# Performance work log

Measured on AMD Instinct MI355X. Metric: run time of the kernel, lower is better.

## Reference

```python
import jax, jax.numpy as jnp
import numpy as np

DIM = 128
K = 4
B, H, W = 2, 256, 256
DEFORM_WEIGHT = 0.3


def conv2d(x, w, b, pad):
    # x [B,C,H,W], w [O,I,kh,kw], stride 1
    y = jax.lax.conv_general_dilated(
        x, w, (1, 1), [(pad, pad), (pad, pad)],
        dimension_numbers=('NCHW', 'OIHW', 'NCHW'))
    return y + b[None, :, None, None]


def gelu(x):
    return jax.nn.gelu(x, approximate=False)  # torch nn.GELU default (erf)


def grid_sample_k(feat, grid):
    """Bilinear grid_sample, padding_mode='border', align_corners=True.
    feat: [B,C,H,W]; grid: [B,K,H,W,2] (x,y) in [-1,1]. Returns [B,C,K,H,W]."""
    Bn, C, Hh, Ww = feat.shape
    px = (grid[..., 0] + 1.0) * 0.5 * (Ww - 1)
    py = (grid[..., 1] + 1.0) * 0.5 * (Hh - 1)
    px = jnp.clip(px, 0.0, Ww - 1)
    py = jnp.clip(py, 0.0, Hh - 1)
    x0 = jnp.floor(px).astype(jnp.int32)
    y0 = jnp.floor(py).astype(jnp.int32)
    x1 = jnp.minimum(x0 + 1, Ww - 1)
    y1 = jnp.minimum(y0 + 1, Hh - 1)
    wx = (px - x0)[:, None]  # [B,1,K,H,W]
    wy = (py - y0)[:, None]
    featf = feat.reshape(Bn, C, Hh * Ww)

    def gather(yi, xi):
        idx = (yi * Ww + xi).reshape(Bn, -1)  # [B, K*H*W]
        g = jax.vmap(lambda f, i: f[:, i])(featf, idx)  # [B,C,K*H*W]
        return g.reshape(Bn, C, *yi.shape[1:])

    v00 = gather(y0, x0)
    v01 = gather(y0, x1)
    v10 = gather(y1, x0)
    v11 = gather(y1, x1)
    return (v00 * (1 - wx) * (1 - wy) + v01 * wx * (1 - wy)
            + v10 * (1 - wx) * wy + v11 * wx * wy)


def setup_inputs() -> dict:
    key = jax.random.key(0)
    ks = jax.random.split(key, 16)
    nrm = lambda k, shape, s: jax.random.normal(k, shape, dtype=jnp.float32) * s
    return {
        'query_feat': jax.random.normal(ks[0], (B, DIM, H, W), dtype=jnp.float32),
        'key_feat': jax.random.normal(ks[1], (B, DIM, H, W), dtype=jnp.float32),
        # offset_net: Conv(dim,dim,3) -> GELU -> Conv(dim,2K,3); small scale keeps offsets sane
        'ow1': nrm(ks[2], (DIM, DIM, 3, 3), 0.02), 'ob1': jnp.zeros((DIM,), jnp.float32),
        'ow2': nrm(ks[3], (2 * K, DIM, 3, 3), 0.01), 'ob2': jnp.zeros((2 * K,), jnp.float32),
        # weight_net: Conv(dim,dim//4,3) -> GELU -> Conv(dim//4,K,1)
        'ww1': nrm(ks[4], (DIM // 4, DIM, 3, 3), 0.05), 'wb1': jnp.zeros((DIM // 4,), jnp.float32),
        'ww2': nrm(ks[5], (K, DIM // 4, 1, 1), 0.05), 'wb2': jnp.zeros((K,), jnp.float32),
        # fusion_conv: Conv(dim,dim,1) -> GELU -> Conv(dim,dim,1)
        'fw1': nrm(ks[6], (DIM, DIM, 1, 1), 0.05), 'fb1': jnp.zeros((DIM,), jnp.float32),
        'fw2': nrm(ks[7], (DIM, DIM, 1, 1), 0.05), 'fb2': jnp.zeros((DIM,), jnp.float32),
    }


def reference(query_feat, key_feat, ow1, ob1, ow2, ob2, ww1, wb1, ww2, wb2,
              fw1, fb1, fw2, fb2):
    offsets = conv2d(gelu(conv2d(query_feat, ow1, ob1, 1)), ow2, ob2, 1)  # [B,2K,H,W]
    wlog = conv2d(gelu(conv2d(query_feat, ww1, wb1, 1)), ww2, wb2, 0)     # [B,K,H,W]
    Bn, C, Hh, Ww = key_feat.shape
    Kp = wlog.shape[1]
    off = offsets.reshape(Bn, Kp, 2, Hh, Ww).transpose(0, 1, 3, 4, 2)  # [B,K,H,W,2]
    gy, gx = jnp.meshgrid(jnp.linspace(-1.0, 1.0, Hh),
                          jnp.linspace(-1.0, 1.0, Ww), indexing='ij')
    base = jnp.stack([gx, gy], axis=-1).astype(off.dtype)  # [H,W,2] (x,y)
    scale = jnp.array([Ww / 2.0, Hh / 2.0], dtype=off.dtype)
    grid = jnp.clip(base + off / scale, -1.0, 1.0)  # [B,K,H,W,2]
    sampled = grid_sample_k(key_feat, grid)  # [B,C,K,H,W]
    wsoft = jax.nn.softmax(wlog, axis=1)[:, None]  # [B,1,K,H,W]
    agg = (sampled * wsoft).sum(axis=2)  # [B,C,H,W]
    fused = conv2d(gelu(conv2d(agg, fw1, fb1, 0)), fw2, fb2, 0)
    return query_feat + fused * DEFORM_WEIGHT
```

## Files before the change

kernel.cpp:

```cpp
#include <hip/hip_runtime.h>
#include <hip/hip_fp16.h>

typedef unsigned short u16;
typedef __attribute__((ext_vector_type(8))) short bf16x8;
typedef __attribute__((ext_vector_type(4))) float f32x4;

constexpr int B_ = 2, C_ = 128, H_ = 256, W_ = 256, P_ = H_ * W_;
constexpr int HP_ = 258, WP_ = 258;

union HU { __half2 h; unsigned int u; };

__device__ __forceinline__ float bf2f(u16 u) {
  union { unsigned int i; float f; } v; v.i = ((unsigned int)u) << 16; return v.f;
}
__device__ __forceinline__ u16 f2bf(float f) {
  union { float f; unsigned int i; } v; v.f = f;
  return (u16)((v.i + 0x7fffu + ((v.i >> 16) & 1u)) >> 16);
}
__device__ __forceinline__ float gelu_f(float x) {
  float u = x * (1.5957691216057308f + 0.071354816272f * x * x);
  return x / (1.0f + __expf(-u));
}

__device__ __forceinline__ void async16(const u16* g, u16* l) {
  __builtin_amdgcn_global_load_lds(
      (const __attribute__((address_space(1))) unsigned int*)g,
      (__attribute__((address_space(3))) unsigned int*)l, 16, 0, 0);
}

__global__ __launch_bounds__(256) void border_zero(u16* __restrict__ buf) {
  int idx = blockIdx.x * 256 + threadIdx.x;
  int c = idx & 127;
  int t = idx >> 7;
  int pos = t % 258;
  int side = (t / 258) & 3;
  int b = t / (258 * 4);
  int h, w;
  if (side == 0) { h = 0;   w = pos; }
  else if (side == 1) { h = 257; w = pos; }
  else if (side == 2) { h = pos; w = 0; }
  else { h = pos; w = 257; }
  buf[(((size_t)b * HP_ + h) * WP_ + w) * C_ + c] = 0;
}

__global__ __launch_bounds__(256) void to_nhwc(const float* __restrict__ in, u16* __restrict__ out,
                                               int OHp, int OWp, int opad) {
  __shared__ u16 l[64 * 66];
  int tid = threadIdx.x;
  int b = blockIdx.z >> 1, c0 = (blockIdx.z & 1) * 64;
  int h = blockIdx.y, w0 = blockIdx.x * 64;
  for (int it = 0; it < 16; ++it) {
    int lin = it * 256 + tid;
    int c = lin >> 6, w = lin & 63;
    l[c * 66 + w] = f2bf(in[(((size_t)b * C_ + c0 + c) * H_ + h) * W_ + w0 + w]);
  }
  __syncthreads();
  for (int it = 0; it < 16; ++it) {
    int lin = it * 256 + tid;
    int w = lin >> 6, c = lin & 63;
    out[(((size_t)b * OHp + h + opad) * OWp + (w0 + w + opad)) * C_ + c0 + c] = l[c * 66 + w];
  }
}

__global__ __launch_bounds__(256) void repack_weights(
    const float* __restrict__ ow1, const float* __restrict__ ow2,
    const float* __restrict__ ww1, const float* __restrict__ fw1,
    const float* __restrict__ fw2, u16* __restrict__ wb) {
  int idx = blockIdx.x * 256 + threadIdx.x;
  float v;
  if (idx < 184320) {
    int e = idx & 7, lr = (idx >> 3) & 15, kb = (idx >> 7) & 3;
    int t = idx >> 9;
    int g = t % 10, u = t / 10;
    int cq = u & 3, tap = u >> 2;
    int ci = cq * 32 + kb * 8 + e, co = g * 16 + lr;
    v = (co < 128) ? ow1[(co * 128 + ci) * 9 + tap]
                   : ww1[((co - 128) * 128 + ci) * 9 + tap];
  } else if (idx < 202752) {
    int j = idx - 184320;
    int e = j & 7, lr = (j >> 3) & 15, kb = (j >> 7) & 3;
    int cq = (j >> 9) & 3, tap = j >> 11;
    int ci = cq * 32 + kb * 8 + e, co = lr;
    v = (co < 8) ? ow2[(co * 128 + ci) * 9 + tap] : 0.0f;
  } else if (idx < 219136) {
    v = fw1[idx - 202752];
  } else {
    v = fw2[idx - 219136];
  }
  wb[idx] = f2bf(v);
}

template <int BM, int BN, int WR, int WC, int GT, int EPI>
__global__ __launch_bounds__(256) void gemm_conv3(
    const u16* __restrict__ A, const u16* __restrict__ Wf,
    const float* __restrict__ bias1, const float* __restrict__ bias2,
    u16* __restrict__ outb, u16* __restrict__ outw, float* __restrict__ outf) {
  constexpr int TM = BM / WR / 16, TN = BN / WC / 16;
  constexpr int RP = BM + 16;
  constexpr int CHR = RP * 4;
  __shared__ __align__(16) u16 As[3 * RP * 32];
  const int tid = threadIdx.x, lane = tid & 63, wave = tid >> 6;
  const int id = blockIdx.x;
  const int s = id >> 3;
  const int h = ((id & 7) << 5) | (s & 31);
  const int w0 = ((s >> 5) & 1) * BM;
  const int b = (s >> 6) & 1;
  const int wm = (wave / WC) * (BM / WR), wn = (wave % WC) * (BN / WC);
  const int lr = lane & 15, kq = lane >> 4;
  const int gbase = wn >> 4;

  int preA[TM][3];
#pragma unroll
  for (int i = 0; i < TM; i++)
#pragma unroll
    for (int kx = 0; kx < 3; kx++) {
      int row = wm + i * 16 + lr + kx;
      preA[i][kx] = row * 64 + (((kq ^ (row >> 1)) & 3) << 4);
    }

  f32x4 acc[TM][TN];
#pragma unroll
  for (int i = 0; i < TM; i++)
#pragma unroll
    for (int j = 0; j < TN; j++) { f32x4 z = {0.f, 0.f, 0.f, 0.f}; acc[i][j] = z; }

  const size_t rowpx = ((size_t)b * HP_ + h) * WP_ + w0;
  for (int cq = 0; cq < 4; ++cq) {
    const int ci0 = cq * 32;
    __syncthreads();
    for (int i = tid; i < 3 * CHR; i += 256) {
      int ky = i / CHR;
      int rem = i - ky * CHR;
      int px = rem >> 2, cb = rem & 3;
      async16(A + (rowpx + (size_t)ky * WP_ + px) * 128 + ci0 + (((cb ^ (px >> 1)) & 3) << 3),
              As + i * 8);
    }
    __syncthreads();
#pragma unroll
    for (int tap = 0; tap < 9; ++tap) {
      const int ky = tap / 3, kx = tap % 3;
      bf16x8 bfr[TN], af[TM];
#pragma unroll
      for (int j = 0; j < TN; ++j)
        bfr[j] = *(const bf16x8*)&Wf[(size_t)((((tap * 4 + cq) * GT + gbase + j) * 4 + kq) * 16 + lr) * 8];
#pragma unroll
      for (int i = 0; i < TM; ++i)
        af[i] = *(const bf16x8*)((const char*)As + ky * (RP * 64) + preA[i][kx]);
#pragma unroll
      for (int i = 0; i < TM; i++)
#pragma unroll
        for (int j = 0; j < TN; j++)
          acc[i][j] = __builtin_amdgcn_mfma_f32_16x16x32_bf16(af[i], bfr[j], acc[i][j], 0, 0, 0);
    }
  }

#pragma unroll
  for (int i = 0; i < TM; i++) {
#pragma unroll
    for (int j = 0; j < TN; j++) {
      const int co = wn + j * 16 + lr;
#pragma unroll
      for (int r = 0; r < 4; r++) {
        const int w = w0 + wm + i * 16 + (lane >> 4) * 4 + r;
        float v = acc[i][j][r];
        if (EPI == 3) {
          if (co < 128) {
            v = gelu_f(v + bias1[co]);
            outb[(((size_t)b * HP_ + h + 1) * WP_ + (w + 1)) * 128 + co] = f2bf(v);
          } else {
            v = gelu_f(v + bias2[co - 128]);
            outw[((size_t)b * P_ + (size_t)h * W_ + w) * 32 + (co - 128)] = f2bf(v);
          }
        } else {
          if (co < 8)
            outf[((size_t)b * P_ + (size_t)h * W_ + w) * 8 + co] = v + bias1[co];
        }
      }
    }
  }
}

template <int BM, int BN, int WR, int WC, int EPI>
__global__ __launch_bounds__(256) void gemm_conv(
    const u16* __restrict__ A, const u16* __restrict__ Wt,
    const float* __restrict__ bias,
    u16* __restrict__ outb, float* __restrict__ outf,
    const float* __restrict__ resid) {
  constexpr int TM = BM / WR / 16, TN = BN / WC / 16;
  __shared__ __align__(16) u16 As[BM * 64];
  __shared__ __align__(16) u16 Bs[BN * 64];
  const int tid = threadIdx.x, lane = tid & 63, wave = tid >> 6;
  const int h = blockIdx.y, w0 = blockIdx.x * BM;
  const int b = blockIdx.z;
  const int wr = wave / WC, wc = wave % WC;
  const int wm = wr * (BM / WR), wn = wc * (BN / WC);
  const int lr = lane & 15;
  const int sw = (lr & 7);

  f32x4 acc[TM][TN];
#pragma unroll
  for (int i = 0; i < TM; i++)
#pragma unroll
    for (int j = 0; j < TN; j++) { f32x4 z = {0.f, 0.f, 0.f, 0.f}; acc[i][j] = z; }

  for (int c = 0; c < 2; ++c) {
    const int ci0 = c << 6;
    const u16* Ab = A + (((size_t)b * H_ + h) * W_ + w0) * 128 + ci0;
    const u16* Wb = Wt + ci0;
    __syncthreads();
    for (int i = tid; i < BM * 8; i += 256) {
      int r = i >> 3, cb = i & 7;
      async16(Ab + r * 128 + ((cb ^ (r & 7)) << 3), As + i * 8);
    }
    for (int i = tid; i < BN * 8; i += 256) {
      int r = i >> 3, cb = i & 7;
      async16(Wb + r * 128 + ((cb ^ (r & 7)) << 3), Bs + i * 8);
    }
    __syncthreads();
#pragma unroll
    for (int ks = 0; ks < 2; ++ks) {
      const int kb = ks * 4 + (lane >> 4);
      bf16x8 af[TM], bfr[TN];
#pragma unroll
      for (int i = 0; i < TM; i++)
        af[i] = *(const bf16x8*)&As[(wm + i * 16 + lr) * 64 + ((kb ^ sw) << 3)];
#pragma unroll
      for (int j = 0; j < TN; j++)
        bfr[j] = *(const bf16x8*)&Bs[(wn + j * 16 + lr) * 64 + ((kb ^ sw) << 3)];
#pragma unroll
      for (int i = 0; i < TM; i++)
#pragma unroll
        for (int j = 0; j < TN; j++)
          acc[i][j] = __builtin_amdgcn_mfma_f32_16x16x32_bf16(af[i], bfr[j], acc[i][j], 0, 0, 0);
    }
  }

#pragma unroll
  for (int i = 0; i < TM; i++) {
#pragma unroll
    for (int j = 0; j < TN; j++) {
      const int co = wn + j * 16 + lr;
      if (EPI == 2) {
        const int w = w0 + wm + i * 16 + (lane >> 4) * 4;
        size_t idx = ((size_t)b * 128 + co) * (size_t)P_ + (size_t)h * W_ + w;
        float4 rv = *(const float4*)&resid[idx];
        float bi = bias[co];
        float4 ov;
        ov.x = rv.x + 0.3f * (acc[i][j][0] + bi);
        ov.y = rv.y + 0.3f * (acc[i][j][1] + bi);
        ov.z = rv.z + 0.3f * (acc[i][j][2] + bi);
        ov.w = rv.w + 0.3f * (acc[i][j][3] + bi);
        *(float4*)&outf[idx] = ov;
      } else {
#pragma unroll
        for (int r = 0; r < 4; r++) {
          const int w = w0 + wm + i * 16 + (lane >> 4) * 4 + r;
          float v = gelu_f(acc[i][j][r] + bias[co]);
          outb[(((size_t)b * H_ + h) * W_ + w) * 128 + co] = f2bf(v);
        }
      }
    }
  }
}

__global__ __launch_bounds__(256) void prep(
    const float* __restrict__ offs, const u16* __restrict__ w1,
    const float* __restrict__ ww2, const float* __restrict__ wb2,
    uint4* __restrict__ desc) {
  const int pix = blockIdx.x * 256 + threadIdx.x;
  const int p = pix & 65535, h = p >> 8, w = p & 255;
  const u16* wp = w1 + (size_t)pix * 32;
  float f[32];
#pragma unroll
  for (int i = 0; i < 32; i += 2) {
    unsigned int u = *(const unsigned int*)&wp[i];
    f[i] = bf2f((u16)u); f[i + 1] = bf2f((u16)(u >> 16));
  }
  float lg[4];
#pragma unroll
  for (int k = 0; k < 4; k++) {
    float s = wb2[k];
#pragma unroll
    for (int i = 0; i < 32; i++) s = fmaf(ww2[k * 32 + i], f[i], s);
    lg[k] = s;
  }
  float mx = fmaxf(fmaxf(lg[0], lg[1]), fmaxf(lg[2], lg[3]));
  float e[4], sum = 0.f;
#pragma unroll
  for (int k = 0; k < 4; k++) { e[k] = __expf(lg[k] - mx); sum += e[k]; }
  const float inv = 1.0f / sum;

  const float* op = offs + (size_t)pix * 8;
#pragma unroll
  for (int k = 0; k < 4; k++) {
    float gx = (2.0f * w / 255.0f - 1.0f) + op[2 * k] * (1.0f / 128.0f);
    float gy = (2.0f * h / 255.0f - 1.0f) + op[2 * k + 1] * (1.0f / 128.0f);
    gx = fminf(fmaxf(gx, -1.f), 1.f);
    gy = fminf(fmaxf(gy, -1.f), 1.f);
    float px = fminf(fmaxf((gx + 1.f) * 127.5f, 0.f), 255.f);
    float py = fminf(fmaxf((gy + 1.f) * 127.5f, 0.f), 255.f);
    int x0 = (int)px, y0 = (int)py;
    int x1 = min(x0 + 1, 255), y1 = min(y0 + 1, 255);
    float wx = px - x0, wy = py - y0;
    float wk = e[k] * inv;
    float w00 = (1.f - wx) * (1.f - wy) * wk, w01 = wx * (1.f - wy) * wk;
    float w10 = (1.f - wx) * wy * wk,         w11 = wx * wy * wk;
    HU t01, t23;
    t01.h = __floats2half2_rn(w00, w01);
    t23.h = __floats2half2_rn(w10, w11);
    uint4 d;
    d.x = (unsigned)(y0 * 256 + x0) | ((unsigned)(x1 - x0) << 16) | ((unsigned)(y1 - y0) << 17);
    d.y = t01.u; d.z = t23.u; d.w = 0;
    desc[(size_t)pix * 4 + k] = d;
  }
}

__global__ __launch_bounds__(256) void sampler(
    const uint4* __restrict__ desc, const u16* __restrict__ keyn, u16* __restrict__ agg) {
  const int tid = threadIdx.x, lane = tid & 63, wv = tid >> 6;
  const int pix = blockIdx.x * 4 + wv;
  const int b = pix >> 16;
  const u16* kb = keyn + (size_t)b * (P_ * C_) + 2 * lane;
  float a0 = 0.f, a1 = 0.f;
#pragma unroll
  for (int k = 0; k < 4; ++k) {
    uint4 d = desc[(size_t)pix * 4 + k];
    const int boff = (int)(d.x & 0xFFFFu) << 7;
    const int o01 = (int)((d.x >> 16) & 1u) << 7;
    const int o10 = (int)((d.x >> 17) & 1u) << 15;
    const u16* c0 = kb + boff;
    unsigned u00 = *(const unsigned*)(c0);
    unsigned u01 = *(const unsigned*)(c0 + o01);
    unsigned u10 = *(const unsigned*)(c0 + o10);
    unsigned u11 = *(const unsigned*)(c0 + o10 + o01);
    HU t01, t23; t01.u = d.y; t23.u = d.z;
    float2 wA = __half22float2(t01.h);
    float2 wB = __half22float2(t23.h);
    a0 = fmaf(wA.x, bf2f((u16)u00), a0);
    a0 = fmaf(wA.y, bf2f((u16)u01), a0);
    a0 = fmaf(wB.x, bf2f((u16)u10), a0);
    a0 = fmaf(wB.y, bf2f((u16)u11), a0);
    a1 = fmaf(wA.x, bf2f((u16)(u00 >> 16)), a1);
    a1 = fmaf(wA.y, bf2f((u16)(u01 >> 16)), a1);
    a1 = fmaf(wB.x, bf2f((u16)(u10 >> 16)), a1);
    a1 = fmaf(wB.y, bf2f((u16)(u11 >> 16)), a1);
  }
  unsigned outu = ((unsigned)f2bf(a1) << 16) | (unsigned)f2bf(a0);
  *(unsigned*)&agg[(size_t)pix * C_ + 2 * lane] = outu;
}

extern "C" void kernel_launch(void* const* d_in, const int* in_sizes, int n_in,
                              void* d_out, int out_size, void* d_ws, size_t ws_size,
                              hipStream_t stream) {
  (void)in_sizes; (void)n_in; (void)out_size; (void)ws_size;
  const float* q   = (const float*)d_in[0];
  const float* key = (const float*)d_in[1];
  const float* ow1 = (const float*)d_in[2];
  const float* ob1 = (const float*)d_in[3];
  const float* ow2 = (const float*)d_in[4];
  const float* ob2 = (const float*)d_in[5];
  const float* ww1 = (const float*)d_in[6];
  const float* wb1 = (const float*)d_in[7];
  const float* ww2 = (const float*)d_in[8];
  const float* wb2 = (const float*)d_in[9];
  const float* fw1 = (const float*)d_in[10];
  const float* fb1 = (const float*)d_in[11];
  const float* fw2 = (const float*)d_in[12];
  const float* fb2 = (const float*)d_in[13];
  float* out = (float*)d_out;
  char* ws = (char*)d_ws;

  u16* qpad   = (u16*)(ws);
  u16* t1pad  = (u16*)(ws + 34080768);
  u16* keyn   = (u16*)(ws + 68161536);
  float* offs = (float*)(ws + 101715968);
  u16* w1b    = (u16*)(ws + 105910272);
  u16* wbuf   = (u16*)(ws + 114298880);
  u16* t2  = qpad;
  u16* agg = t1pad;
  uint4* desc = (uint4*)(ws + 16777216);

  border_zero<<<1032, 256, 0, stream>>>(qpad);
  border_zero<<<1032, 256, 0, stream>>>(t1pad);
  repack_weights<<<920, 256, 0, stream>>>(ow1, ow2, ww1, fw1, fw2, wbuf);
  to_nhwc<<<dim3(4, 256, 4), 256, 0, stream>>>(q, qpad, HP_, WP_, 1);
  to_nhwc<<<dim3(4, 256, 4), 256, 0, stream>>>(key, keyn, H_, W_, 0);

  gemm_conv3<128, 160, 2, 2, 10, 3><<<1024, 256, 0, stream>>>(
      qpad, wbuf, ob1, wb1, t1pad, w1b, nullptr);
  gemm_conv3<128, 16, 4, 1, 1, 1><<<1024, 256, 0, stream>>>(
      t1pad, wbuf + 184320, ob2, nullptr, nullptr, nullptr, offs);
  prep<<<512, 256, 0, stream>>>(offs, w1b, ww2, wb2, desc);
  sampler<<<32768, 256, 0, stream>>>(desc, keyn, agg);
  gemm_conv<128, 128, 2, 2, 0><<<dim3(2, 256, 2), 256, 0, stream>>>(
      agg, wbuf + 202752, fb1, t2, nullptr, nullptr);
  gemm_conv<128, 128, 2, 2, 2><<<dim3(2, 256, 2), 256, 0, stream>>>(
      t2, wbuf + 219136, fb2, nullptr, out, q);
}
```

Before: 397.5 us.

## Fuse prologue kernels, retile 3x3 conv, fuse offset conv with prep and 1x1 pair

Merges border zeroing, NHWC conversion and weight repacking into one launch. Retiles the big 3x3 conv to 4-row by 32-pixel tiles so halo rows are reused across output rows. Fuses the offset conv with the softmax/descriptor prep through LDS, removing the fp32 offsets round trip. Fuses both 1x1 convs so the GELU intermediate stays in LDS instead of global memory. The larger LDS footprint may lower occupancy.

```diff
diff --git a/kernel.cpp b/kernel.cpp
--- a/kernel.cpp
+++ b/kernel.cpp
@@ -28,273 +28,259 @@
       (__attribute__((address_space(3))) unsigned int*)l, 16, 0, 0);
 }
 
-__global__ __launch_bounds__(256) void border_zero(u16* __restrict__ buf) {
-  int idx = blockIdx.x * 256 + threadIdx.x;
-  int c = idx & 127;
-  int t = idx >> 7;
-  int pos = t % 258;
-  int side = (t / 258) & 3;
-  int b = t / (258 * 4);
-  int h, w;
-  if (side == 0) { h = 0;   w = pos; }
-  else if (side == 1) { h = 257; w = pos; }
-  else if (side == 2) { h = pos; w = 0; }
-  else { h = pos; w = 257; }
-  buf[(((size_t)b * HP_ + h) * WP_ + w) * C_ + c] = 0;
-}
-
-__global__ __launch_bounds__(256) void to_nhwc(const float* __restrict__ in, u16* __restrict__ out,
-                                               int OHp, int OWp, int opad) {
-  __shared__ u16 l[64 * 66];
-  int tid = threadIdx.x;
-  int b = blockIdx.z >> 1, c0 = (blockIdx.z & 1) * 64;
-  int h = blockIdx.y, w0 = blockIdx.x * 64;
-  for (int it = 0; it < 16; ++it) {
-    int lin = it * 256 + tid;
-    int c = lin >> 6, w = lin & 63;
-    l[c * 66 + w] = f2bf(in[(((size_t)b * C_ + c0 + c) * H_ + h) * W_ + w0 + w]);
-  }
-  __syncthreads();
-  for (int it = 0; it < 16; ++it) {
-    int lin = it * 256 + tid;
-    int w = lin >> 6, c = lin & 63;
-    out[(((size_t)b * OHp + h + opad) * OWp + (w0 + w + opad)) * C_ + c0 + c] = l[c * 66 + w];
-  }
-}
-
-__global__ __launch_bounds__(256) void repack_weights(
+__global__ __launch_bounds__(256) void prologue(
+    const float* __restrict__ q, const float* __restrict__ key,
     const float* __restrict__ ow1, const float* __restrict__ ow2,
     const float* __restrict__ ww1, const float* __restrict__ fw1,
-    const float* __restrict__ fw2, u16* __restrict__ wb) {
-  int idx = blockIdx.x * 256 + threadIdx.x;
-  float v;
-  if (idx < 184320) {
-    int e = idx & 7, lr = (idx >> 3) & 15, kb = (idx >> 7) & 3;
-    int t = idx >> 9;
-    int g = t % 10, u = t / 10;
-    int cq = u & 3, tap = u >> 2;
-    int ci = cq * 32 + kb * 8 + e, co = g * 16 + lr;
-    v = (co < 128) ? ow1[(co * 128 + ci) * 9 + tap]
-                   : ww1[((co - 128) * 128 + ci) * 9 + tap];
-  } else if (idx < 202752) {
-    int j = idx - 184320;
-    int e = j & 7, lr = (j >> 3) & 15, kb = (j >> 7) & 3;
-    int cq = (j >> 9) & 3, tap = j >> 11;
-    int ci = cq * 32 + kb * 8 + e, co = lr;
-    v = (co < 8) ? ow2[(co * 128 + ci) * 9 + tap] : 0.0f;
-  } else if (idx < 219136) {
-    v = fw1[idx - 202752];
+    const float* __restrict__ fw2,
+    u16* __restrict__ qpad, u16* __restrict__ keyn, u16* __restrict__ t1pad,
+    u16* __restrict__ wb) {
+  __shared__ u16 l[64 * 66];
+  const int id = blockIdx.x, tid = threadIdx.x;
+  if (id < 8192) {
+    int z = id >> 10, r = id & 1023;
+    int bx = r & 3, by = r >> 2;
+    const float* in; u16* out; int OW, opad;
+    if (z < 4) { in = q; out = qpad; OW = WP_; opad = 1; }
+    else { z -= 4; in = key; out = keyn; OW = W_; opad = 0; }
+    int b = z >> 1, c0 = (z & 1) * 64;
+    int h = by, w0 = bx * 64;
+    for (int it = 0; it < 16; ++it) {
+      int lin = it * 256 + tid;
+      int c = lin >> 6, w = lin & 63;
+      l[c * 66 + w] = f2bf(in[(((size_t)b * C_ + c0 + c) * H_ + h) * W_ + w0 + w]);
+    }
+    __syncthreads();
+    int OH = (opad ? HP_ : H_);
+    for (int it = 0; it < 16; ++it) {
+      int lin = it * 256 + tid;
+      int w = lin >> 6, c = lin & 63;
+      out[(((size_t)b * OH + h + opad) * OW + (w0 + w + opad)) * C_ + c0 + c] = l[c * 66 + w];
+    }
+  } else if (id < 10256) {
+    int j = id - 8192;
+    u16* buf = (j < 1032) ? qpad : t1pad;
+    int idx = ((j < 1032) ? j : j - 1032) * 256 + tid;
+    int c = idx & 127;
+    int t = idx >> 7;
+    int pos = t % 258;
+    int side = (t / 258) & 3;
+    int b = t / (258 * 4);
+    int h, w;
+    if (side == 0) { h = 0; w = pos; }
+    else if (side == 1) { h = 257; w = pos; }
+    else if (side == 2) { h = pos; w = 0; }
+    else { h = pos; w = 257; }
+    buf[(((size_t)b * HP_ + h) * WP_ + w) * C_ + c] = 0;
   } else {
-    v = fw2[idx - 219136];
-  }
-  wb[idx] = f2bf(v);
-}
-
-template <int BM, int BN, int WR, int WC, int GT, int EPI>
-__global__ __launch_bounds__(256) void gemm_conv3(
+    int idx = (id - 10256) * 256 + tid;
+    float v;
+    if (idx < 184320) {
+      int e = idx & 7, lr = (idx >> 3) & 15, kb = (idx >> 7) & 3;
+      int t = idx >> 9;
+      int g = t % 10, u = t / 10;
+      int cq = u & 3, tap = u >> 2;
+      int ci = cq * 32 + kb * 8 + e, co = g * 16 + lr;
+      v = (co < 128) ? ow1[(co * 128 + ci) * 9 + tap]
+                     : ww1[((co - 128) * 128 + ci) * 9 + tap];
+    } else if (idx < 202752) {
+      int j = idx - 184320;
+      int e = j & 7, lr = (j >> 3) & 15, kb = (j >> 7) & 3;
+      int cq = (j >> 9) & 3, tap = j >> 11;
+      int ci = cq * 32 + kb * 8 + e, co = lr;
+      v = (co < 8) ? ow2[(co * 128 + ci) * 9 + tap] : 0.0f;
+    } else if (idx < 219136) {
+      v = fw1[idx - 202752];
+    } else {
+      v = fw2[idx - 219136];
+    }
+    wb[idx] = f2bf(v);
+  }
+}
+
+__global__ __launch_bounds__(256) void conv3_big(
     const u16* __restrict__ A, const u16* __restrict__ Wf,
     const float* __restrict__ bias1, const float* __restrict__ bias2,
-    u16* __restrict__ outb, u16* __restrict__ outw, float* __restrict__ outf) {
-  constexpr int TM = BM / WR / 16, TN = BN / WC / 16;
-  constexpr int RP = BM + 16;
-  constexpr int CHR = RP * 4;
-  __shared__ __align__(16) u16 As[3 * RP * 32];
+    u16* __restrict__ outb, u16* __restrict__ outw) {
+  constexpr int RPX = 36, ROWU = RPX * 32;
+  __shared__ __align__(16) u16 As[6 * ROWU];
   const int tid = threadIdx.x, lane = tid & 63, wave = tid >> 6;
   const int id = blockIdx.x;
   const int s = id >> 3;
-  const int h = ((id & 7) << 5) | (s & 31);
-  const int w0 = ((s >> 5) & 1) * BM;
-  const int b = (s >> 6) & 1;
-  const int wm = (wave / WC) * (BM / WR), wn = (wave % WC) * (BN / WC);
+  const int h0 = (((id & 7) << 3) | (s & 7)) << 2;
+  const int w0 = ((s >> 3) & 7) << 5;
+  const int b = s >> 6;
+  const int wr = wave >> 1, wc = wave & 1;
+  const int wm = wr * 64, wn = wc * 80;
   const int lr = lane & 15, kq = lane >> 4;
   const int gbase = wn >> 4;
 
-  int preA[TM][3];
-#pragma unroll
-  for (int i = 0; i < TM; i++)
+  int rbase[4], pxb[4], preA[4][3];
+#pragma unroll
+  for (int i = 0; i < 4; i++) {
+    rbase[i] = (wm + i * 16) >> 5;
+    pxb[i] = (wm + i * 16) & 31;
 #pragma unroll
     for (int kx = 0; kx < 3; kx++) {
-      int row = wm + i * 16 + lr + kx;
-      preA[i][kx] = row * 64 + (((kq ^ (row >> 1)) & 3) << 4);
-    }
-
-  f32x4 acc[TM][TN];
-#pragma unroll
-  for (int i = 0; i < TM; i++)
-#pragma unroll
-    for (int j = 0; j < TN; j++) { f32x4 z = {0.f, 0.f, 0.f, 0.f}; acc[i][j] = z; }
-
-  const size_t rowpx = ((size_t)b * HP_ + h) * WP_ + w0;
+      int pxv = pxb[i] + lr + kx;
+      preA[i][kx] = (pxv * 4 + (kq ^ ((pxv >> 1) & 3))) * 8;
+    }
+  }
+
+  f32x4 acc[4][5];
+#pragma unroll
+  for (int i = 0; i < 4; i++)
+#pragma unroll
+    for (int j = 0; j < 5; j++) { f32x4 z = {0.f, 0.f, 0.f, 0.f}; acc[i][j] = z; }
+
   for (int cq = 0; cq < 4; ++cq) {
     const int ci0 = cq * 32;
     __syncthreads();
-    for (int i = tid; i < 3 * CHR; i += 256) {
-      int ky = i / CHR;
-      int rem = i - ky * CHR;
-      int px = rem >> 2, cb = rem & 3;
-      async16(A + (rowpx + (size_t)ky * WP_ + px) * 128 + ci0 + (((cb ^ (px >> 1)) & 3) << 3),
+    for (int i = tid; i < 864; i += 256) {
+      int ry = i / 144;
+      int rem = i - ry * 144;
+      int px = rem >> 2, c8 = rem & 3;
+      int g = c8 ^ ((px >> 1) & 3);
+      async16(A + ((size_t)(b * HP_ + h0 + ry) * WP_ + (w0 + px)) * 128 + ci0 + g * 8,
               As + i * 8);
     }
     __syncthreads();
 #pragma unroll
     for (int tap = 0; tap < 9; ++tap) {
       const int ky = tap / 3, kx = tap % 3;
-      bf16x8 bfr[TN], af[TM];
-#pragma unroll
-      for (int j = 0; j < TN; ++j)
-        bfr[j] = *(const bf16x8*)&Wf[(size_t)((((tap * 4 + cq) * GT + gbase + j) * 4 + kq) * 16 + lr) * 8];
-#pragma unroll
-      for (int i = 0; i < TM; ++i)
-        af[i] = *(const bf16x8*)((const char*)As + ky * (RP * 64) + preA[i][kx]);
-#pragma unroll
-      for (int i = 0; i < TM; i++)
-#pragma unroll
-        for (int j = 0; j < TN; j++)
+      bf16x8 bfr[5], af[4];
+#pragma unroll
+      for (int j = 0; j < 5; ++j)
+        bfr[j] = *(const bf16x8*)&Wf[(size_t)((((tap * 4 + cq) * 10 + gbase + j) * 4 + kq) * 16 + lr) * 8];
+#pragma unroll
+      for (int i = 0; i < 4; ++i)
+        af[i] = *(const bf16x8*)&As[(rbase[i] + ky) * ROWU + preA[i][kx]];
+#pragma unroll
+      for (int i = 0; i < 4; i++)
+#pragma unroll
+        for (int j = 0; j < 5; j++)
           acc[i][j] = __builtin_amdgcn_mfma_f32_16x16x32_bf16(af[i], bfr[j], acc[i][j], 0, 0, 0);
     }
   }
 
 #pragma unroll
-  for (int i = 0; i < TM; i++) {
-#pragma unroll
-    for (int j = 0; j < TN; j++) {
+  for (int i = 0; i < 4; i++) {
+    const int h = h0 + rbase[i];
+#pragma unroll
+    for (int j = 0; j < 5; j++) {
       const int co = wn + j * 16 + lr;
 #pragma unroll
       for (int r = 0; r < 4; r++) {
-        const int w = w0 + wm + i * 16 + (lane >> 4) * 4 + r;
+        const int w = w0 + pxb[i] + (lane >> 4) * 4 + r;
         float v = acc[i][j][r];
-        if (EPI == 3) {
-          if (co < 128) {
-            v = gelu_f(v + bias1[co]);
-            outb[(((size_t)b * HP_ + h + 1) * WP_ + (w + 1)) * 128 + co] = f2bf(v);
-          } else {
-            v = gelu_f(v + bias2[co - 128]);
-            outw[((size_t)b * P_ + (size_t)h * W_ + w) * 32 + (co - 128)] = f2bf(v);
-          }
+        if (co < 128) {
+          v = gelu_f(v + bias1[co]);
+          outb[(((size_t)b * HP_ + h + 1) * WP_ + (w + 1)) * 128 + co] = f2bf(v);
         } else {
-          if (co < 8)
-            outf[((size_t)b * P_ + (size_t)h * W_ + w) * 8 + co] = v + bias1[co];
+          v = gelu_f(v + bias2[co - 128]);
+          outw[((size_t)b * P_ + (size_t)h * W_ + w) * 32 + (co - 128)] = f2bf(v);
         }
       }
     }
   }
 }
 
-template <int BM, int BN, int WR, int WC, int EPI>
-__global__ __launch_bounds__(256) void gemm_conv(
-    const u16* __restrict__ A, const u16* __restrict__ Wt,
+__global__ __launch_bounds__(256) void conv_off(
+    const u16* __restrict__ A, const u16* __restrict__ Wf,
     const float* __restrict__ bias,
-    u16* __restrict__ outb, float* __restrict__ outf,
-    const float* __restrict__ resid) {
-  constexpr int TM = BM / WR / 16, TN = BN / WC / 16;
-  __shared__ __align__(16) u16 As[BM * 64];
-  __shared__ __align__(16) u16 Bs[BN * 64];
+    const u16* __restrict__ w1b, const float* __restrict__ ww2,
+    const float* __restrict__ wb2, uint4* __restrict__ desc) {
+  constexpr int RPX = 66, ROWU = RPX * 32;
+  __shared__ __align__(16) u16 As[6 * ROWU];
+  float* off_lds = (float*)As;
   const int tid = threadIdx.x, lane = tid & 63, wave = tid >> 6;
-  const int h = blockIdx.y, w0 = blockIdx.x * BM;
-  const int b = blockIdx.z;
-  const int wr = wave / WC, wc = wave % WC;
-  const int wm = wr * (BM / WR), wn = wc * (BN / WC);
-  const int lr = lane & 15;
-  const int sw = (lr & 7);
-
-  f32x4 acc[TM][TN];
-#pragma unroll
-  for (int i = 0; i < TM; i++)
-#pragma unroll
-    for (int j = 0; j < TN; j++) { f32x4 z = {0.f, 0.f, 0.f, 0.f}; acc[i][j] = z; }
-
-  for (int c = 0; c < 2; ++c) {
-    const int ci0 = c << 6;
-    const u16* Ab = A + (((size_t)b * H_ + h) * W_ + w0) * 128 + ci0;
-    const u16* Wb = Wt + ci0;
-    __syncthreads();
-    for (int i = tid; i < BM * 8; i += 256) {
-      int r = i >> 3, cb = i & 7;
-      async16(Ab + r * 128 + ((cb ^ (r & 7)) << 3), As + i * 8);
-    }
-    for (int i = tid; i < BN * 8; i += 256) {
-      int r = i >> 3, cb = i & 7;
-      async16(Wb + r * 128 + ((cb ^ (r & 7)) << 3), Bs + i * 8);
-    }
-    __syncthreads();
-#pragma unroll
-    for (int ks = 0; ks < 2; ++ks) {
-      const int kb = ks * 4 + (lane >> 4);
-      bf16x8 af[TM], bfr[TN];
-#pragma unroll
-      for (int i = 0; i < TM; i++)
-        af[i] = *(const bf16x8*)&As[(wm + i * 16 + lr) * 64 + ((kb ^ sw) << 3)];
-#pragma unroll
-      for (int j = 0; j < TN; j++)
-        bfr[j] = *(const bf16x8*)&Bs[(wn + j * 16 + lr) * 64 + ((kb ^ sw) << 3)];
-#pragma unroll
-      for (int i = 0; i < TM; i++)
-#pragma unroll
-        for (int j = 0; j < TN; j++)
-          acc[i][j] = __builtin_amdgcn_mfma_f32_16x16x32_bf16(af[i], bfr[j], acc[i][j], 0, 0, 0);
-    }
-  }
-
-#pragma unroll
-  for (int i = 0; i < TM; i++) {
-#pragma unroll
-    for (int j = 0; j < TN; j++) {
-      const int co = wn + j * 16 + lr;
-      if (EPI == 2) {
-        const int w = w0 + wm + i * 16 + (lane >> 4) * 4;
-        size_t idx = ((size_t)b * 128 + co) * (size_t)P_ + (size_t)h * W_ + w;
-        float4 rv = *(const float4*)&resid[idx];
-        float bi = bias[co];
-        float4 ov;
-        ov.x = rv.x + 0.3f * (acc[i][j][0] + bi);
-        ov.y = rv.y + 0.3f * (acc[i][j][1] + bi);
-        ov.z = rv.z + 0.3f * (acc[i][j][2] + bi);
-        ov.w = rv.w + 0.3f * (acc[i][j][3] + bi);
-        *(float4*)&outf[idx] = ov;
-      } else {
-#pragma unroll
-        for (int r = 0; r < 4; r++) {
-          const int w = w0 + wm + i * 16 + (lane >> 4) * 4 + r;
-          float v = gelu_f(acc[i][j][r] + bias[co]);
-          outb[(((size_t)b * H_ + h) * W_ + w) * 128 + co] = f2bf(v);
-        }
+  const int id = blockIdx.x;
+  const int s = id >> 3;
+  const int h0 = (((id & 7) << 3) | (s & 7)) << 2;
+  const int w0 = ((s >> 3) & 3) << 6;
+  const int b = s >> 5;
+  const int lr = lane & 15, kq = lane >> 4;
+
+  int preA[4][3];
+#pragma unroll
+  for (int i = 0; i < 4; i++)
+#pragma unroll
+    for (int kx = 0; kx < 3; kx++) {
+      int pxv = i * 16 + lr + kx;
+      preA[i][kx] = (pxv * 4 + (kq ^ ((pxv >> 1) & 3))) * 8;
+    }
+
+  f32x4 acc[4];
+#pragma unroll
+  for (int i = 0; i < 4; i++) { f32x4 z = {0.f, 0.f, 0.f, 0.f}; acc[i] = z; }
+
+  for (int cq = 0; cq < 4; ++cq) {
+    const int ci0 = cq * 32;
+    __syncthreads();
+    for (int i = tid; i < 1584; i += 256) {
+      int ry = i / 264;
+      int rem = i - ry * 264;
+      int px = rem >> 2, c8 = rem & 3;
+      int g = c8 ^ ((px >> 1) & 3);
+      async16(A + ((size_t)(b * HP_ + h0 + ry) * WP_ + (w0 + px)) * 128 + ci0 + g * 8,
+              As + i * 8);
+    }
+    __syncthreads();
+#pragma unroll
+    for (int tap = 0; tap < 9; ++tap) {
+      const int ky = tap / 3, kx = tap % 3;
+      bf16x8 bw = *(const bf16x8*)&Wf[(size_t)(((tap * 4 + cq) * 4 + kq) * 16 + lr) * 8];
+      bf16x8 af[4];
+#pragma unroll
+      for (int i = 0; i < 4; ++i)
+        af[i] = *(const bf16x8*)&As[(wave + ky) * ROWU + preA[i][kx]];
+#pragma unroll
+      for (int i = 0; i < 4; i++)
+        acc[i] = __builtin_amdgcn_mfma_f32_16x16x32_bf16(af[i], bw, acc[i], 0, 0, 0);
+    }
+  }
+
+  __syncthreads();
+#pragma unroll
+  for (int i = 0; i < 4; i++) {
+#pragma unroll
+    for (int r = 0; r < 4; r++) {
+      if (lr < 8) {
+        int px = i * 16 + (lane >> 4) * 4 + r;
+        off_lds[(wave * 64 + px) * 9 + lr] = acc[i][r] + bias[lr];
       }
     }
   }
-}
-
-__global__ __launch_bounds__(256) void prep(
-    const float* __restrict__ offs, const u16* __restrict__ w1,
-    const float* __restrict__ ww2, const float* __restrict__ wb2,
-    uint4* __restrict__ desc) {
-  const int pix = blockIdx.x * 256 + threadIdx.x;
-  const int p = pix & 65535, h = p >> 8, w = p & 255;
-  const u16* wp = w1 + (size_t)pix * 32;
+  __syncthreads();
+
+  const int pp = tid;
+  const int h = h0 + (pp >> 6), w = w0 + (pp & 63);
+  const int pix = b * P_ + h * W_ + w;
+  const u16* wp = w1b + (size_t)pix * 32;
   float f[32];
 #pragma unroll
   for (int i = 0; i < 32; i += 2) {
-    unsigned int u = *(const unsigned int*)&wp[i];
+    unsigned u = *(const unsigned*)&wp[i];
     f[i] = bf2f((u16)u); f[i + 1] = bf2f((u16)(u >> 16));
   }
   float lg[4];
 #pragma unroll
   for (int k = 0; k < 4; k++) {
-    float s = wb2[k];
-#pragma unroll
-    for (int i = 0; i < 32; i++) s = fmaf(ww2[k * 32 + i], f[i], s);
-    lg[k] = s;
+    float sacc = wb2[k];
+#pragma unroll
+    for (int i = 0; i < 32; i++) sacc = fmaf(ww2[k * 32 + i], f[i], sacc);
+    lg[k] = sacc;
   }
   float mx = fmaxf(fmaxf(lg[0], lg[1]), fmaxf(lg[2], lg[3]));
   float e[4], sum = 0.f;
 #pragma unroll
   for (int k = 0; k < 4; k++) { e[k] = __expf(lg[k] - mx); sum += e[k]; }
   const float inv = 1.0f / sum;
-
-  const float* op = offs + (size_t)pix * 8;
 #pragma unroll
   for (int k = 0; k < 4; k++) {
-    float gx = (2.0f * w / 255.0f - 1.0f) + op[2 * k] * (1.0f / 128.0f);
-    float gy = (2.0f * h / 255.0f - 1.0f) + op[2 * k + 1] * (1.0f / 128.0f);
+    float ox = off_lds[pp * 9 + 2 * k], oy = off_lds[pp * 9 + 2 * k + 1];
+    float gx = (2.0f * w / 255.0f - 1.0f) + ox * (1.0f / 128.0f);
+    float gy = (2.0f * h / 255.0f - 1.0f) + oy * (1.0f / 128.0f);
     gx = fminf(fmaxf(gx, -1.f), 1.f);
     gy = fminf(fmaxf(gy, -1.f), 1.f);
     float px = fminf(fmaxf((gx + 1.f) * 127.5f, 0.f), 255.f);
@@ -349,6 +335,121 @@
   *(unsigned*)&agg[(size_t)pix * C_ + 2 * lane] = outu;
 }
 
+__global__ __launch_bounds__(256) void conv_fuse(
+    const u16* __restrict__ Aagg, const u16* __restrict__ W1, const u16* __restrict__ W2,
+    const float* __restrict__ b1, const float* __restrict__ b2,
+    const float* __restrict__ resid, float* __restrict__ out) {
+  __shared__ __align__(16) u16 SM[16384];
+  __shared__ __align__(16) u16 T2[128 * 136];
+  u16* As = SM;
+  u16* Bs = SM + 8192;
+  const int tid = threadIdx.x, lane = tid & 63, wave = tid >> 6;
+  const int h = blockIdx.y, w0 = blockIdx.x * 128;
+  const int b = blockIdx.z;
+  const int wr = wave >> 1, wc = wave & 1;
+  const int wm = wr * 64, wn = wc * 64;
+  const int lr = lane & 15, kq = lane >> 4;
+  const int sw = lr & 7;
+
+  f32x4 acc[4][4];
+#pragma unroll
+  for (int i = 0; i < 4; i++)
+#pragma unroll
+    for (int j = 0; j < 4; j++) { f32x4 z = {0.f, 0.f, 0.f, 0.f}; acc[i][j] = z; }
+
+  for (int c = 0; c < 2; ++c) {
+    const int ci0 = c << 6;
+    const u16* Ab = Aagg + (((size_t)b * H_ + h) * W_ + w0) * 128 + ci0;
+    const u16* Wb = W1 + ci0;
+    __syncthreads();
+    for (int i = tid; i < 128 * 8; i += 256) {
+      int r = i >> 3, cb = i & 7;
+      async16(Ab + r * 128 + ((cb ^ (r & 7)) << 3), As + i * 8);
+    }
+    for (int i = tid; i < 128 * 8; i += 256) {
+      int r = i >> 3, cb = i & 7;
+      async16(Wb + r * 128 + ((cb ^ (r & 7)) << 3), Bs + i * 8);
+    }
+    __syncthreads();
+#pragma unroll
+    for (int ks = 0; ks < 2; ++ks) {
+      const int kb = ks * 4 + kq;
+      bf16x8 af[4], bfr[4];
+#pragma unroll
+      for (int i = 0; i < 4; i++)
+        af[i] = *(const bf16x8*)&As[(wm + i * 16 + lr) * 64 + ((kb ^ sw) << 3)];
+#pragma unroll
+      for (int j = 0; j < 4; j++)
+        bfr[j] = *(const bf16x8*)&Bs[(wn + j * 16 + lr) * 64 + ((kb ^ sw) << 3)];
+#pragma unroll
+      for (int i = 0; i < 4; i++)
+#pragma unroll
+        for (int j = 0; j < 4; j++)
+          acc[i][j] = __builtin_amdgcn_mfma_f32_16x16x32_bf16(af[i], bfr[j], acc[i][j], 0, 0, 0);
+    }
+  }
+
+#pragma unroll
+  for (int i = 0; i < 4; i++)
+#pragma unroll
+    for (int j = 0; j < 4; j++) {
+      const int co = wn + j * 16 + lr;
+#pragma unroll
+      for (int r = 0; r < 4; r++) {
+        const int px = wm + i * 16 + (lane >> 4) * 4 + r;
+        T2[px * 136 + co] = f2bf(gelu_f(acc[i][j][r] + b1[co]));
+      }
+    }
+  __syncthreads();
+  for (int i = tid; i < 2048; i += 256) {
+    int r = i >> 4, sl = i & 15;
+    int g = sl ^ (r & 7);
+    async16(W2 + r * 128 + g * 8, SM + i * 8);
+  }
+  __syncthreads();
+
+#pragma unroll
+  for (int i = 0; i < 4; i++)
+#pragma unroll
+    for (int j = 0; j < 4; j++) { f32x4 z = {0.f, 0.f, 0.f, 0.f}; acc[i][j] = z; }
+#pragma unroll
+  for (int ks = 0; ks < 4; ++ks) {
+    const int kc = ks * 4 + kq;
+    bf16x8 af[4], bfr[4];
+#pragma unroll
+    for (int i = 0; i < 4; i++)
+      af[i] = *(const bf16x8*)&T2[(wm + i * 16 + lr) * 136 + kc * 8];
+#pragma unroll
+    for (int j = 0; j < 4; j++) {
+      int rr = wn + j * 16 + lr;
+      bfr[j] = *(const bf16x8*)&SM[rr * 128 + (kc ^ (rr & 7)) * 8];
+    }
+#pragma unroll
+    for (int i = 0; i < 4; i++)
+#pragma unroll
+      for (int j = 0; j < 4; j++)
+        acc[i][j] = __builtin_amdgcn_mfma_f32_16x16x32_bf16(af[i], bfr[j], acc[i][j], 0, 0, 0);
+  }
+
+#pragma unroll
+  for (int i = 0; i < 4; i++) {
+#pragma unroll
+    for (int j = 0; j < 4; j++) {
+      const int co = wn + j * 16 + lr;
+      const int w = w0 + wm + i * 16 + (lane >> 4) * 4;
+      size_t idx = ((size_t)b * 128 + co) * (size_t)P_ + (size_t)h * W_ + w;
+      float4 rv = *(const float4*)&resid[idx];
+      float bi = b2[co];
+      float4 ov;
+      ov.x = rv.x + 0.3f * (acc[i][j][0] + bi);
+      ov.y = rv.y + 0.3f * (acc[i][j][1] + bi);
+      ov.z = rv.z + 0.3f * (acc[i][j][2] + bi);
+      ov.w = rv.w + 0.3f * (acc[i][j][3] + bi);
+      *(float4*)&out[idx] = ov;
+    }
+  }
+}
+
 extern "C" void kernel_launch(void* const* d_in, const int* in_sizes, int n_in,
                               void* d_out, int out_size, void* d_ws, size_t ws_size,
                               hipStream_t stream) {
@@ -370,30 +471,19 @@
   float* out = (float*)d_out;
   char* ws = (char*)d_ws;
 
-  u16* qpad   = (u16*)(ws);
-  u16* t1pad  = (u16*)(ws + 34080768);
-  u16* keyn   = (u16*)(ws + 68161536);
-  float* offs = (float*)(ws + 101715968);
-  u16* w1b    = (u16*)(ws + 105910272);
-  u16* wbuf   = (u16*)(ws + 114298880);
-  u16* t2  = qpad;
+  u16* qpad  = (u16*)(ws);
+  u16* t1pad = (u16*)(ws + 34080768);
+  u16* keyn  = (u16*)(ws + 68161536);
+  u16* w1b   = (u16*)(ws + 101715968);
+  u16* wbuf  = (u16*)(ws + 110104576);
+  uint4* desc = (uint4*)ws;
   u16* agg = t1pad;
-  uint4* desc = (uint4*)(ws + 16777216);
-
-  border_zero<<<1032, 256, 0, stream>>>(qpad);
-  border_zero<<<1032, 256, 0, stream>>>(t1pad);
-  repack_weights<<<920, 256, 0, stream>>>(ow1, ow2, ww1, fw1, fw2, wbuf);
-  to_nhwc<<<dim3(4, 256, 4), 256, 0, stream>>>(q, qpad, HP_, WP_, 1);
-  to_nhwc<<<dim3(4, 256, 4), 256, 0, stream>>>(key, keyn, H_, W_, 0);
-
-  gemm_conv3<128, 160, 2, 2, 10, 3><<<1024, 256, 0, stream>>>(
-      qpad, wbuf, ob1, wb1, t1pad, w1b, nullptr);
-  gemm_conv3<128, 16, 4, 1, 1, 1><<<1024, 256, 0, stream>>>(
-      t1pad, wbuf + 184320, ob2, nullptr, nullptr, nullptr, offs);
-  prep<<<512, 256, 0, stream>>>(offs, w1b, ww2, wb2, desc);
+
+  prologue<<<11176, 256, 0, stream>>>(q, key, ow1, ow2, ww1, fw1, fw2,
+                                      qpad, keyn, t1pad, wbuf);
+  conv3_big<<<1024, 256, 0, stream>>>(qpad, wbuf, ob1, wb1, t1pad, w1b);
+  conv_off<<<512, 256, 0, stream>>>(t1pad, wbuf + 184320, ob2, w1b, ww2, wb2, desc);
   sampler<<<32768, 256, 0, stream>>>(desc, keyn, agg);
-  gemm_conv<128, 128, 2, 2, 0><<<dim3(2, 256, 2), 256, 0, stream>>>(
-      agg, wbuf + 202752, fb1, t2, nullptr, nullptr);
-  gemm_conv<128, 128, 2, 2, 2><<<dim3(2, 256, 2), 256, 0, stream>>>(
-      t2, wbuf + 219136, fb2, nullptr, out, q);
-}
+  conv_fuse<<<dim3(2, 256, 2), 256, 0, stream>>>(agg, wbuf + 202752, wbuf + 219136,
+                                                 fb1, fb2, q, out);
+}
```

Measured after the change: 357.6 us. 1.11x faster.
